# Optimization experiments

Hardware: AMD Instinct MI355X
Metric: run time of the kernel (lower is better)

## Reference

```python
import jax, jax.numpy as jnp
import numpy as np

C = 256          # in_channels
CI = 128         # inter_channels = C // reduction
N_B, H, W = 4, 64, 64


def setup_inputs() -> dict:
    key = jax.random.key(0)
    ks = jax.random.split(key, 9)
    std = 0.01
    inp = {
        "x": jax.random.normal(ks[0], (N_B, C, H, W), dtype=jnp.float32),
        # 1x1 conv weights stored as [out_ch, in_ch]
        "w_g": jax.random.normal(ks[1], (CI, C), dtype=jnp.float32) * std,
        "b_g": jnp.zeros((CI,), dtype=jnp.float32),
        "w_theta": jax.random.normal(ks[2], (CI, C), dtype=jnp.float32) * std,
        "b_theta": jnp.zeros((CI,), dtype=jnp.float32),
        "w_phi": jax.random.normal(ks[3], (CI, C), dtype=jnp.float32) * std,
        "b_phi": jnp.zeros((CI,), dtype=jnp.float32),
        # conv_out: use small random instead of exact zeros so output is non-trivial
        "w_out": jax.random.normal(ks[4], (C, CI), dtype=jnp.float32) * std,
        "b_out": jnp.zeros((C,), dtype=jnp.float32),
    }
    return inp


def reference(x, w_g, b_g, w_theta, b_theta, w_phi, b_phi, w_out, b_out):
    n, c, h, w = x.shape
    nhw = h * w
    xf = x.reshape(n, c, nhw)                                   # [n, C, N]
    # 1x1 convs == channel matmuls
    g_x = jnp.einsum('ncs,oc->nso', xf, w_g) + b_g              # [n, N, CI]
    theta_x = jnp.einsum('ncs,oc->nso', xf, w_theta) + b_theta  # [n, N, CI]
    phi_x = jnp.einsum('ncs,oc->nos', xf, w_phi) + b_phi[None, :, None]  # [n, CI, N]
    # pairwise weights: [n, N, N]
    pw = jnp.einsum('nqc,ncs->nqs', theta_x, phi_x)
    # faithful to original: DIVIDE by d**-0.5 (i.e. multiply by sqrt(d))
    pw = pw / (theta_x.shape[-1] ** (-0.5))
    pw = jax.nn.softmax(pw, axis=-1)
    y = jnp.einsum('nqs,nsc->nqc', pw, g_x)                     # [n, N, CI]
    y = y.transpose(0, 2, 1).reshape(n, -1, h, w)               # [n, CI, H, W]
    out = jnp.einsum('nchw,oc->nohw', y, w_out) + b_out[None, :, None, None]
    return x + out
```

## Files before the change

kernel.cpp:

```cpp
#include <hip/hip_runtime.h>
#include <cmath>

typedef __attribute__((ext_vector_type(8))) short bf16x8;
typedef __attribute__((ext_vector_type(4))) short bf16x4;
typedef __attribute__((ext_vector_type(4))) float f32x4;

#define MFMA16(a,b,c)  __builtin_amdgcn_mfma_f32_16x16x32_bf16((a),(b),(c),0,0,0)
#define MFMA16K16(a,b,c) __builtin_amdgcn_mfma_f32_16x16x16bf16_1k((a),(b),(c),0,0,0)

#if __has_builtin(__builtin_amdgcn_exp2f)
#define EXP2F(x) __builtin_amdgcn_exp2f(x)
#else
#define EXP2F(x) exp2f(x)
#endif

#define KSCALE 16.3222312f

#define NB 4
#define CH 256
#define CI 128
#define NS 4096

__device__ __forceinline__ unsigned short f2bf(float f) {
    unsigned int u = __builtin_bit_cast(unsigned int, f);
    u += 0x7fffu + ((u >> 16) & 1u);
    return (unsigned short)(u >> 16);
}
__device__ __forceinline__ unsigned int pk2(float lo, float hi) {
    return (unsigned int)f2bf(lo) | ((unsigned int)f2bf(hi) << 16);
}
__device__ __forceinline__ unsigned int pk2t(float lo, float hi) {
    unsigned int ul = __builtin_bit_cast(unsigned int, lo);
    unsigned int uh = __builtin_bit_cast(unsigned int, hi);
    return (uh & 0xffff0000u) | (ul >> 16);
}
__device__ __forceinline__ float bf2f(unsigned int ush) {
    return __builtin_bit_cast(float, ush << 16);
}

__device__ __forceinline__ void gload16(void* lds, const void* g) {
    __builtin_amdgcn_global_load_lds(
        (const __attribute__((address_space(1))) unsigned int*)g,
        (__attribute__((address_space(3))) unsigned int*)lds,
        16, 0, 0);
}

__global__ void wcvt_kernel(const float* __restrict__ w_g, const float* __restrict__ w_th,
                            const float* __restrict__ w_ph, const float* __restrict__ w_out,
                            const float* __restrict__ b_g, const float* __restrict__ b_th,
                            const float* __restrict__ b_ph,
                            unsigned short* __restrict__ wbf, float* __restrict__ bsc) {
    int i = blockIdx.x * 256 + threadIdx.x;
    float v;
    if (i < 32768)        v = w_g[i];
    else if (i < 65536)   v = w_th[i - 32768] * KSCALE;
    else if (i < 98304)   v = w_ph[i - 65536];
    else                  v = w_out[i - 98304];
    wbf[i] = f2bf(v);
    if (i < 128)          bsc[i] = b_g[i];
    else if (i < 256)     bsc[i] = b_th[i - 128] * KSCALE;
    else if (i < 384)     bsc[i] = b_ph[i - 256];
}

__global__ __launch_bounds__(512, 2)
void proj_kernel(const float* __restrict__ x,
                 const unsigned short* __restrict__ wbf, const float* __restrict__ bsc,
                 unsigned short* __restrict__ theta,
                 unsigned short* __restrict__ phi,
                 unsigned short* __restrict__ gT) {
    const int tid  = threadIdx.x;
    const int wid  = tid >> 6;
    const int lane = tid & 63;
    const int quad = lane >> 4;
    const int l15  = lane & 15;
    const int stile = blockIdx.x;
    const int n     = blockIdx.y;
    const int s0    = stile * 64;

    const float* xN = x + (size_t)n * CH * NS;

    __shared__ unsigned int xp[64 * 128];

#pragma unroll
    for (int i = 0; i < 4; i++) {
        int t  = i * 512 + tid;
        int s4 = t & 15;
        int cp = t >> 4;
        const float* p0 = xN + (size_t)(2 * cp) * NS + s0 + s4 * 4;
        float4 a = *(const float4*)p0;
        float4 b = *(const float4*)(p0 + NS);
        int col = (((cp >> 2) ^ (s4 & 7)) << 2) | (cp & 3);
        unsigned int* xr = xp + (s4 * 4) * 128 + col;
        xr[0]   = pk2(a.x, b.x);
        xr[128] = pk2(a.y, b.y);
        xr[256] = pk2(a.z, b.z);
        xr[384] = pk2(a.w, b.w);
    }
    __syncthreads();

    const int srow = (wid & 3) * 16 + l15;
    const int oh   = wid >> 2;
    const int sw7  = (srow >> 2) & 7;
#pragma unroll
    for (int wi = 0; wi < 3; wi++) {
        f32x4 acc[4];
#pragma unroll
        for (int ot = 0; ot < 4; ot++) acc[ot] = (f32x4){0.f, 0.f, 0.f, 0.f};
        const unsigned short* W = wbf + (size_t)wi * 32768 + (size_t)oh * 64 * CH;
#pragma unroll
        for (int kc = 0; kc < 8; kc++) {
            bf16x8 af = *(const bf16x8*)(&xp[srow * 128 + (((kc * 4 + quad) ^ sw7) << 2)]);
#pragma unroll
            for (int ot = 0; ot < 4; ot++) {
                bf16x8 wf = *(const bf16x8*)(W + (size_t)(ot * 16 + l15) * CH + kc * 32 + quad * 8);
                acc[ot] = MFMA16(af, wf, acc[ot]);
            }
        }
        const float* Bv = bsc + wi * 128 + oh * 64;
#pragma unroll
        for (int ot = 0; ot < 4; ot++) {
            int o = oh * 64 + ot * 16 + l15;
            float bias = Bv[ot * 16 + l15];
#pragma unroll
            for (int r = 0; r < 4; r++) {
                int sg = s0 + (wid & 3) * 16 + quad * 4 + r;
                float v = acc[ot][r] + bias;
                if (wi == 0)
                    gT[((size_t)n * CI + o) * NS + sg] = f2bf(v);
                else if (wi == 1)
                    theta[((size_t)n * NS + sg) * CI + o] = f2bf(v);
                else
                    phi[((size_t)n * NS + sg) * CI + o] = f2bf(v);
            }
        }
    }
}

__global__ __launch_bounds__(256, 2)
void attn_kernel(const unsigned short* __restrict__ theta,
                 const unsigned short* __restrict__ phi,
                 const unsigned short* __restrict__ gT,
                 unsigned short* __restrict__ Opart,
                 float* __restrict__ lbuf) {
    const int tid  = threadIdx.x;
    const int wid  = tid >> 6;
    const int lane = tid & 63;
    const int quad = lane >> 4;
    const int l15  = lane & 15;
    const int sn    = blockIdx.x;
    const int split = sn >> 2;
    const int n     = sn & 3;
    const int qb    = blockIdx.y;
    const int qbase = qb * 128 + wid * 32;

    const unsigned short* thN = theta + (size_t)n * NS * CI;
    const unsigned short* phN = phi   + (size_t)n * NS * CI;
    const unsigned short* gN  = gT    + (size_t)n * CI * NS;

    __shared__ unsigned short smem[32768];
    unsigned short* Kb = smem;
    unsigned short* Vb = smem + 16384;

    bf16x8 qf[2][4];
#pragma unroll
    for (int qt = 0; qt < 2; qt++)
#pragma unroll
        for (int kc = 0; kc < 4; kc++)
            qf[qt][kc] = *(const bf16x8*)(thN + (size_t)(qbase + qt * 16 + l15) * CI + kc * 32 + quad * 8);

    f32x4 O[8][2];
#pragma unroll
    for (int ct = 0; ct < 8; ct++)
#pragma unroll
        for (int qt = 0; qt < 2; qt++) O[ct][qt] = (f32x4){0.f, 0.f, 0.f, 0.f};
    float lrun[2] = {0.f, 0.f};

    const int sbase0 = split * 1024;
    const int lh16 = lane >> 4, lm16 = lane & 15;
    const int lh8  = lane >> 3, lm8  = lane & 7;

#pragma unroll
    for (int i = 0; i < 4; i++) {
        int seg = wid * 4 + i;
        int s   = seg * 4 + lh16;
        int j   = lm16 ^ (s & 15);
        gload16(Kb + seg * 512, phN + (size_t)(sbase0 + s) * CI + j * 8);
    }
#pragma unroll
    for (int i = 0; i < 4; i++) {
        int seg = wid * 4 + i;
        int c   = seg * 8 + lh8;
        int j   = lm8 ^ (c & 7);
        gload16(Vb + seg * 512, gN + (size_t)c * NS + sbase0 + j * 8);
    }

    for (int ck = 0; ck < 16; ck++) {
        const int cur = ck & 1, nxt = cur ^ 1;
        unsigned short* Kc = Kb + cur * 8192;
        unsigned short* Vc = Vb + cur * 8192;
        __syncthreads();

        if (ck + 1 < 16) {
            const int sb1 = sbase0 + (ck + 1) * 64;
#pragma unroll
            for (int i = 0; i < 4; i++) {
                int seg = wid * 4 + i;
                int s   = seg * 4 + lh16;
                int j   = lm16 ^ (s & 15);
                gload16(Kb + nxt * 8192 + seg * 512, phN + (size_t)(sb1 + s) * CI + j * 8);
            }
#pragma unroll
            for (int i = 0; i < 4; i++) {
                int seg = wid * 4 + i;
                int c   = seg * 8 + lh8;
                int j   = lm8 ^ (c & 7);
                gload16(Vb + nxt * 8192 + seg * 512, gN + (size_t)c * NS + sb1 + j * 8);
            }
        }

        f32x4 S[2][4];
#pragma unroll
        for (int qt = 0; qt < 2; qt++)
#pragma unroll
            for (int st = 0; st < 4; st++) S[qt][st] = (f32x4){0.f, 0.f, 0.f, 0.f};
        __builtin_amdgcn_s_setprio(1);
#pragma unroll
        for (int st = 0; st < 4; st++) {
#pragma unroll
            for (int kc = 0; kc < 4; kc++) {
                int s = st * 16 + l15;
                bf16x8 kf = *(const bf16x8*)(Kc + s * 128 + ((kc * 4 + quad) ^ l15) * 8);
#pragma unroll
                for (int qt = 0; qt < 2; qt++)
                    S[qt][st] = MFMA16(kf, qf[qt][kc], S[qt][st]);
            }
        }
        __builtin_amdgcn_s_setprio(0);

        bf16x4 pa[2][4];
#pragma unroll
        for (int qt = 0; qt < 2; qt++) {
            float rsl = 0.f;
#pragma unroll
            for (int st = 0; st < 4; st++) {
                float p0 = EXP2F(S[qt][st][0]);
                float p1 = EXP2F(S[qt][st][1]);
                float p2 = EXP2F(S[qt][st][2]);
                float p3 = EXP2F(S[qt][st][3]);
                rsl += (p0 + p1) + (p2 + p3);
                union { unsigned int uu[2]; bf16x4 v; } pkv;
                pkv.uu[0] = pk2t(p0, p1);
                pkv.uu[1] = pk2t(p2, p3);
                pa[qt][st] = pkv.v;
            }
            lrun[qt] += rsl;
        }

        __builtin_amdgcn_s_setprio(1);
#pragma unroll
        for (int st = 0; st < 4; st++) {
            const int g = (st * 2 + (quad >> 1)) ^ (l15 & 7);
            const int so = g * 8 + (quad & 1) * 4;
#pragma unroll
            for (int ct = 0; ct < 8; ct++) {
                bf16x4 vf = *(const bf16x4*)(Vc + (ct * 16 + l15) * 64 + so);
#pragma unroll
                for (int qt = 0; qt < 2; qt++)
                    O[ct][qt] = MFMA16K16(vf, pa[qt][st], O[ct][qt]);
            }
        }
        __builtin_amdgcn_s_setprio(0);
    }

    __syncthreads();
    float* tb = (float*)smem + wid * 2048;
    const size_t obase = ((size_t)(split * NB + n)) * NS * CI;
#pragma unroll
    for (int qt = 0; qt < 2; qt++) {
#pragma unroll
        for (int ct = 0; ct < 8; ct++) {
            int p = (ct * 4 + quad) ^ l15;
            *(f32x4*)(tb + l15 * 128 + p * 4) = O[ct][qt];
        }
#pragma unroll
        for (int i = 0; i < 4; i++) {
            int flat = i * 64 + lane;
            int row = flat >> 4, jj = flat & 15;
            f32x4 a = *(const f32x4*)(tb + row * 128 + ((jj * 2) ^ row) * 4);
            f32x4 b = *(const f32x4*)(tb + row * 128 + ((jj * 2 + 1) ^ row) * 4);
            int q = qbase + qt * 16 + row;
            uint4 pkv;
            pkv.x = pk2(a[0], a[1]); pkv.y = pk2(a[2], a[3]);
            pkv.z = pk2(b[0], b[1]); pkv.w = pk2(b[2], b[3]);
            *(uint4*)(Opart + obase + (size_t)q * CI + jj * 8) = pkv;
        }
        __syncthreads();
    }
    lrun[0] += __shfl_xor(lrun[0], 16); lrun[0] += __shfl_xor(lrun[0], 32);
    lrun[1] += __shfl_xor(lrun[1], 16); lrun[1] += __shfl_xor(lrun[1], 32);
    if (quad == 0) {
#pragma unroll
        for (int qt = 0; qt < 2; qt++) {
            int q = qbase + qt * 16 + l15;
            lbuf[(split * NB + n) * NS + q] = lrun[qt];
        }
    }
}

__global__ __launch_bounds__(256, 4)
void outproj_kernel(const float* __restrict__ x,
                    const unsigned short* __restrict__ wbf,
                    const float* __restrict__ b_out,
                    const unsigned short* __restrict__ Opart,
                    const float* __restrict__ lbuf,
                    float* __restrict__ out) {
    const int tid  = threadIdx.x;
    const int wid  = tid >> 6;
    const int lane = tid & 63;
    const int quad = lane >> 4;
    const int l15  = lane & 15;
    const int oh = blockIdx.y;
    const int n  = blockIdx.z;
    const int sw = blockIdx.x * 64 + wid * 16;
    const int T  = NB * NS;

    const int srow = n * NS + sw + l15;
    float l = 0.f;
#pragma unroll
    for (int k = 0; k < 4; k++) l += lbuf[k * T + srow];
    float rinv = 1.0f / l;

    bf16x8 yb[4];
#pragma unroll
    for (int kc = 0; kc < 4; kc++) {
        float f0 = 0.f, f1 = 0.f, f2 = 0.f, f3 = 0.f;
        float f4 = 0.f, f5 = 0.f, f6 = 0.f, f7 = 0.f;
#pragma unroll
        for (int k = 0; k < 4; k++) {
            uint4 v = *(const uint4*)(Opart + ((size_t)k * T + srow) * CI + kc * 32 + quad * 8);
            f0 += bf2f(v.x & 0xffffu); f1 += bf2f(v.x >> 16);
            f2 += bf2f(v.y & 0xffffu); f3 += bf2f(v.y >> 16);
            f4 += bf2f(v.z & 0xffffu); f5 += bf2f(v.z >> 16);
            f6 += bf2f(v.w & 0xffffu); f7 += bf2f(v.w >> 16);
        }
        union { unsigned int uu[4]; bf16x8 vv; } r;
        r.uu[0] = pk2(f0 * rinv, f1 * rinv);
        r.uu[1] = pk2(f2 * rinv, f3 * rinv);
        r.uu[2] = pk2(f4 * rinv, f5 * rinv);
        r.uu[3] = pk2(f6 * rinv, f7 * rinv);
        yb[kc] = r.vv;
    }

    const unsigned short* wob = wbf + 3 * 32768 + (size_t)oh * 128 * CI;
    f32x4 acc[8];
#pragma unroll
    for (int ot = 0; ot < 8; ot++) acc[ot] = (f32x4){0.f, 0.f, 0.f, 0.f};
#pragma unroll
    for (int kc = 0; kc < 4; kc++) {
#pragma unroll
        for (int ot = 0; ot < 8; ot++) {
            bf16x8 wa = *(const bf16x8*)(wob + (size_t)(ot * 16 + l15) * CI + kc * 32 + quad * 8);
            acc[ot] = MFMA16(wa, yb[kc], acc[ot]);
        }
    }
#pragma unroll
    for (int ot = 0; ot < 8; ot++) {
#pragma unroll
        for (int r = 0; r < 4; r++) {
            int o = oh * 128 + ot * 16 + quad * 4 + r;
            size_t idx = ((size_t)n * CH + o) * NS + sw + l15;
            out[idx] = x[idx] + acc[ot][r] + b_out[o];
        }
    }
}

extern "C" void kernel_launch(void* const* d_in, const int* in_sizes, int n_in,
                              void* d_out, int out_size, void* d_ws, size_t ws_size,
                              hipStream_t stream) {
    const float* x     = (const float*)d_in[0];
    const float* w_g   = (const float*)d_in[1];
    const float* b_g   = (const float*)d_in[2];
    const float* w_th  = (const float*)d_in[3];
    const float* b_th  = (const float*)d_in[4];
    const float* w_ph  = (const float*)d_in[5];
    const float* b_ph  = (const float*)d_in[6];
    const float* w_out = (const float*)d_in[7];
    const float* b_out = (const float*)d_in[8];
    float* out = (float*)d_out;

    char* ws = (char*)d_ws;
    unsigned short* theta = (unsigned short*)(ws + 0);
    unsigned short* phi   = (unsigned short*)(ws + 4194304);
    unsigned short* gT    = (unsigned short*)(ws + 8388608);
    unsigned short* Opart = (unsigned short*)(ws + 12582912);
    float* lbuf  = (float*)(ws + 29360128);
    unsigned short* wbf = (unsigned short*)(ws + 29622272);
    float* bsc   = (float*)(ws + 29884416);

    wcvt_kernel<<<512, 256, 0, stream>>>(w_g, w_th, w_ph, w_out, b_g, b_th, b_ph, wbf, bsc);
    proj_kernel<<<dim3(64, NB), 512, 0, stream>>>(x, wbf, bsc, theta, phi, gT);
    attn_kernel<<<dim3(16, 32), 256, 0, stream>>>(theta, phi, gT, Opart, lbuf);
    outproj_kernel<<<dim3(64, 2, NB), 256, 0, stream>>>(x, wbf, b_out, Opart, lbuf, out);
}
```

Measured before the change: 167.7 us.

## Switch attention kernel to 32x32x16 MFMA with permlane-swap P packing

The attention inner loops move from 16x16 MFMA tiles (16x16x32 for S, 16x16x16 for PV) to 32x32x16 bf16 MFMA for both QK^T and PV. The exp'd probabilities are packed with v_perm and rearranged across lane halves with v_permlane32_swap, so the S accumulator layout can feed the PV MFMA B operand directly. The goal is fewer MFMA issues and fewer LDS fragment reads per tile, with wider 8-element V loads. The epilogue is rewritten for the 32x32 accumulator layout and drops the per-pass __syncthreads. The cost is more live accumulator registers per lane, and correctness depends on the lane permutation matching the MFMA operand layout.

Result: faster. 160.4 us (-4.3%).

```diff
diff --git a/kernel.cpp b/kernel.cpp
--- a/kernel.cpp
+++ b/kernel.cpp
@@ -2,11 +2,11 @@
 #include <cmath>
 
 typedef __attribute__((ext_vector_type(8))) short bf16x8;
-typedef __attribute__((ext_vector_type(4))) short bf16x4;
 typedef __attribute__((ext_vector_type(4))) float f32x4;
+typedef __attribute__((ext_vector_type(16))) float f32x16;
 
 #define MFMA16(a,b,c)  __builtin_amdgcn_mfma_f32_16x16x32_bf16((a),(b),(c),0,0,0)
-#define MFMA16K16(a,b,c) __builtin_amdgcn_mfma_f32_16x16x16bf16_1k((a),(b),(c),0,0,0)
+#define MFMA32(a,b,c)  __builtin_amdgcn_mfma_f32_32x32x16_bf16((a),(b),(c),0,0,0)
 
 #if __has_builtin(__builtin_amdgcn_exp2f)
 #define EXP2F(x) __builtin_amdgcn_exp2f(x)
@@ -29,13 +29,23 @@
 __device__ __forceinline__ unsigned int pk2(float lo, float hi) {
     return (unsigned int)f2bf(lo) | ((unsigned int)f2bf(hi) << 16);
 }
-__device__ __forceinline__ unsigned int pk2t(float lo, float hi) {
-    unsigned int ul = __builtin_bit_cast(unsigned int, lo);
-    unsigned int uh = __builtin_bit_cast(unsigned int, hi);
-    return (uh & 0xffff0000u) | (ul >> 16);
+__device__ __forceinline__ unsigned int pkt(float lo, float hi) {
+    return __builtin_amdgcn_perm(__builtin_bit_cast(unsigned int, hi),
+                                 __builtin_bit_cast(unsigned int, lo), 0x07060302u);
 }
 __device__ __forceinline__ float bf2f(unsigned int ush) {
     return __builtin_bit_cast(float, ush << 16);
+}
+
+__device__ __forceinline__ void plswap(unsigned int& wLow, unsigned int& wHigh) {
+    asm volatile("v_permlane32_swap_b32 %0, %1" : "+v"(wLow), "+v"(wHigh));
+}
+
+__device__ __forceinline__ f32x16 zero16() {
+    f32x16 v;
+#pragma unroll
+    for (int i = 0; i < 16; i++) v[i] = 0.f;
+    return v;
 }
 
 __device__ __forceinline__ void gload16(void* lds, const void* g) {
@@ -145,8 +155,8 @@
     const int tid  = threadIdx.x;
     const int wid  = tid >> 6;
     const int lane = tid & 63;
-    const int quad = lane >> 4;
-    const int l15  = lane & 15;
+    const int l31  = lane & 31;
+    const int lh32 = lane >> 5;
     const int sn    = blockIdx.x;
     const int split = sn >> 2;
     const int n     = sn & 3;
@@ -161,19 +171,15 @@
     unsigned short* Kb = smem;
     unsigned short* Vb = smem + 16384;
 
-    bf16x8 qf[2][4];
-#pragma unroll
-    for (int qt = 0; qt < 2; qt++)
-#pragma unroll
-        for (int kc = 0; kc < 4; kc++)
-            qf[qt][kc] = *(const bf16x8*)(thN + (size_t)(qbase + qt * 16 + l15) * CI + kc * 32 + quad * 8);
-
-    f32x4 O[8][2];
-#pragma unroll
-    for (int ct = 0; ct < 8; ct++)
-#pragma unroll
-        for (int qt = 0; qt < 2; qt++) O[ct][qt] = (f32x4){0.f, 0.f, 0.f, 0.f};
-    float lrun[2] = {0.f, 0.f};
+    bf16x8 qf[8];
+#pragma unroll
+    for (int kc = 0; kc < 8; kc++)
+        qf[kc] = *(const bf16x8*)(thN + (size_t)(qbase + l31) * CI + kc * 16 + lh32 * 8);
+
+    f32x16 O[4];
+#pragma unroll
+    for (int ct = 0; ct < 4; ct++) O[ct] = zero16();
+    float lrun = 0.f;
 
     const int sbase0 = split * 1024;
     const int lh16 = lane >> 4, lm16 = lane & 15;
@@ -218,55 +224,53 @@
             }
         }
 
-        f32x4 S[2][4];
-#pragma unroll
-        for (int qt = 0; qt < 2; qt++)
-#pragma unroll
-            for (int st = 0; st < 4; st++) S[qt][st] = (f32x4){0.f, 0.f, 0.f, 0.f};
+        f32x16 S[2];
+        S[0] = zero16(); S[1] = zero16();
         __builtin_amdgcn_s_setprio(1);
 #pragma unroll
-        for (int st = 0; st < 4; st++) {
-#pragma unroll
-            for (int kc = 0; kc < 4; kc++) {
-                int s = st * 16 + l15;
-                bf16x8 kf = *(const bf16x8*)(Kc + s * 128 + ((kc * 4 + quad) ^ l15) * 8);
-#pragma unroll
-                for (int qt = 0; qt < 2; qt++)
-                    S[qt][st] = MFMA16(kf, qf[qt][kc], S[qt][st]);
+        for (int sb = 0; sb < 2; sb++) {
+#pragma unroll
+            for (int kc = 0; kc < 8; kc++) {
+                int s = sb * 32 + l31;
+                bf16x8 kf = *(const bf16x8*)(Kc + s * 128 + (((kc * 2 + lh32) ^ (s & 15)) * 8));
+                S[sb] = MFMA32(kf, qf[kc], S[sb]);
             }
         }
         __builtin_amdgcn_s_setprio(0);
 
-        bf16x4 pa[2][4];
-#pragma unroll
-        for (int qt = 0; qt < 2; qt++) {
-            float rsl = 0.f;
-#pragma unroll
-            for (int st = 0; st < 4; st++) {
-                float p0 = EXP2F(S[qt][st][0]);
-                float p1 = EXP2F(S[qt][st][1]);
-                float p2 = EXP2F(S[qt][st][2]);
-                float p3 = EXP2F(S[qt][st][3]);
-                rsl += (p0 + p1) + (p2 + p3);
-                union { unsigned int uu[2]; bf16x4 v; } pkv;
-                pkv.uu[0] = pk2t(p0, p1);
-                pkv.uu[1] = pk2t(p2, p3);
-                pa[qt][st] = pkv.v;
-            }
-            lrun[qt] += rsl;
-        }
+        bf16x8 pf[4];
+        float lsum = 0.f;
+#pragma unroll
+        for (int ks = 0; ks < 4; ks++) {
+            const int sb = ks >> 1, b = ks & 1;
+            float pA[4], pB[4];
+#pragma unroll
+            for (int m = 0; m < 4; m++) {
+                pA[m] = EXP2F(S[sb][(2 * b) * 4 + m]);
+                pB[m] = EXP2F(S[sb][(2 * b + 1) * 4 + m]);
+            }
+            lsum += ((pA[0] + pA[1]) + (pA[2] + pA[3]))
+                  + ((pB[0] + pB[1]) + (pB[2] + pB[3]));
+            unsigned int wA0 = pkt(pA[0], pA[1]);
+            unsigned int wA1 = pkt(pA[2], pA[3]);
+            unsigned int wB0 = pkt(pB[0], pB[1]);
+            unsigned int wB1 = pkt(pB[2], pB[3]);
+            plswap(wA0, wB0);
+            plswap(wA1, wB1);
+            union { unsigned int u[4]; bf16x8 v; } P;
+            P.u[0] = wA0; P.u[1] = wA1; P.u[2] = wB0; P.u[3] = wB1;
+            pf[ks] = P.v;
+        }
+        lrun += lsum;
 
         __builtin_amdgcn_s_setprio(1);
 #pragma unroll
-        for (int st = 0; st < 4; st++) {
-            const int g = (st * 2 + (quad >> 1)) ^ (l15 & 7);
-            const int so = g * 8 + (quad & 1) * 4;
-#pragma unroll
-            for (int ct = 0; ct < 8; ct++) {
-                bf16x4 vf = *(const bf16x4*)(Vc + (ct * 16 + l15) * 64 + so);
-#pragma unroll
-                for (int qt = 0; qt < 2; qt++)
-                    O[ct][qt] = MFMA16K16(vf, pa[qt][st], O[ct][qt]);
+        for (int ks = 0; ks < 4; ks++) {
+#pragma unroll
+            for (int ct = 0; ct < 4; ct++) {
+                int c = ct * 32 + l31;
+                bf16x8 vf = *(const bf16x8*)(Vc + c * 64 + (((ks * 2 + lh32) ^ (c & 7)) * 8));
+                O[ct] = MFMA32(vf, pf[ks], O[ct]);
             }
         }
         __builtin_amdgcn_s_setprio(0);
@@ -276,35 +280,34 @@
     float* tb = (float*)smem + wid * 2048;
     const size_t obase = ((size_t)(split * NB + n)) * NS * CI;
 #pragma unroll
-    for (int qt = 0; qt < 2; qt++) {
-#pragma unroll
-        for (int ct = 0; ct < 8; ct++) {
-            int p = (ct * 4 + quad) ^ l15;
-            *(f32x4*)(tb + l15 * 128 + p * 4) = O[ct][qt];
-        }
-#pragma unroll
-        for (int i = 0; i < 4; i++) {
-            int flat = i * 64 + lane;
-            int row = flat >> 4, jj = flat & 15;
-            f32x4 a = *(const f32x4*)(tb + row * 128 + ((jj * 2) ^ row) * 4);
-            f32x4 b = *(const f32x4*)(tb + row * 128 + ((jj * 2 + 1) ^ row) * 4);
-            int q = qbase + qt * 16 + row;
-            uint4 pkv;
-            pkv.x = pk2(a[0], a[1]); pkv.y = pk2(a[2], a[3]);
-            pkv.z = pk2(b[0], b[1]); pkv.w = pk2(b[2], b[3]);
-            *(uint4*)(Opart + obase + (size_t)q * CI + jj * 8) = pkv;
-        }
-        __syncthreads();
-    }
-    lrun[0] += __shfl_xor(lrun[0], 16); lrun[0] += __shfl_xor(lrun[0], 32);
-    lrun[1] += __shfl_xor(lrun[1], 16); lrun[1] += __shfl_xor(lrun[1], 32);
-    if (quad == 0) {
-#pragma unroll
-        for (int qt = 0; qt < 2; qt++) {
-            int q = qbase + qt * 16 + l15;
-            lbuf[(split * NB + n) * NS + q] = lrun[qt];
-        }
-    }
+    for (int pass = 0; pass < 2; pass++) {
+#pragma unroll
+        for (int cti = 0; cti < 2; cti++) {
+            const int ct = pass * 2 + cti;
+#pragma unroll
+            for (int g = 0; g < 4; g++) {
+                const int c_local = cti * 32 + 8 * g + 4 * lh32;
+                const int slot = (c_local >> 2) ^ (l31 & 15);
+                f32x4 v;
+                v[0] = O[ct][4 * g + 0]; v[1] = O[ct][4 * g + 1];
+                v[2] = O[ct][4 * g + 2]; v[3] = O[ct][4 * g + 3];
+                *(f32x4*)(tb + l31 * 64 + slot * 4) = v;
+            }
+        }
+#pragma unroll
+        for (int i = 0; i < 8; i++) {
+            const int qr  = i * 4 + (lane >> 4);
+            const int lin = lane & 15;
+            f32x4 v = *(const f32x4*)(tb + qr * 64 + ((lin ^ (qr & 15)) * 4));
+            uint2 w;
+            w.x = pk2(v[0], v[1]);
+            w.y = pk2(v[2], v[3]);
+            *(uint2*)(Opart + obase + (size_t)(qbase + qr) * CI + pass * 64 + lin * 4) = w;
+        }
+    }
+    lrun += __shfl_xor(lrun, 32);
+    if (lane < 32)
+        lbuf[(split * NB + n) * NS + qbase + l31] = lrun;
 }
 
 __global__ __launch_bounds__(256, 4)
```
